# Performance work log

Hardware: AMD Instinct MI355X
Metric: run time of the kernel (lower is better)

Reference implementation:

```python
import jax, jax.numpy as jnp
import numpy as np

WINDOW = 5  # window_size from init


def _avg_pool3d(x, k):
    # Matches F.avg_pool3d(kernel=k, stride=1, padding=k//2,
    # count_include_pad=True): windowed sum with zero padding / k^3.
    pad = k // 2
    s = jax.lax.reduce_window(
        x, 0.0, jax.lax.add,
        window_dimensions=(1, 1, k, k, k),
        window_strides=(1, 1, 1, 1, 1),
        padding=[(0, 0), (0, 0), (pad, pad), (pad, pad), (pad, pad)],
    )
    return s / float(k ** 3)


def setup_inputs() -> dict:
    key = jax.random.key(0)
    k1, k2 = jax.random.split(key)
    shape = (2, 1, 160, 192, 192)  # [B, C, D, H, W]
    source = jax.random.normal(k1, shape, dtype=jnp.float32)
    target = jax.random.normal(k2, shape, dtype=jnp.float32)
    return {"source": source, "target": target}


def reference(source, target):
    conv = lambda x: _avg_pool3d(x, WINDOW)
    src_mean = conv(source)
    tgt_mean = conv(target)
    src_var = conv(source * source) - src_mean * src_mean
    tgt_var = conv(target * target) - tgt_mean * tgt_mean
    cross = conv(source * target) - src_mean * tgt_mean
    lncc = cross * cross / (src_var * tgt_var + 1e-5)
    loss = 1.0 - jnp.mean(lncc)
    return jnp.nan_to_num(loss, nan=1.0, posinf=1.0, neginf=1.0)
```

## Files before the change

### kernel.cpp

```cpp
#include <hip/hip_runtime.h>
#include <math.h>

#define W_ 192
#define H_ 192
#define D_ 160
#define B_ 2
#define TILE 16
#define HALO 20
#define CHUNK 20
#define PLANES (CHUNK + 4)
#define NTOT 11796480.0f

struct Q { float ss, tt, s2, t2, st; };

__global__ __launch_bounds__(256) void lncc_main(const float* __restrict__ src,
                                                 const float* __restrict__ tgt,
                                                 float* __restrict__ acc) {
    __shared__ float2 raw[HALO][HALO + 1];
    __shared__ float4 rs4[HALO][TILE + 1];
    __shared__ float  rs1[HALO][TILE + 1];
    __shared__ float  wsum[4];

    const int tx  = threadIdx.x, ty = threadIdx.y;
    const int tid = ty * TILE + tx;
    const int bz  = blockIdx.z;
    const int b   = bz >> 3;
    const int z0  = (bz & 7) * CHUNK;
    const int bx0 = blockIdx.x * TILE - 2;
    const int by0 = blockIdx.y * TILE - 2;

    Q r0 = {0,0,0,0,0}, r1 = {0,0,0,0,0}, r2 = {0,0,0,0,0},
      r3 = {0,0,0,0,0}, r4 = {0,0,0,0,0};
    Q zs = {0,0,0,0,0};
    float lsum = 0.0f;

    for (int i = 0; i < PLANES; ++i) {
        const int zp = z0 - 2 + i;
        Q ys = {0,0,0,0,0};
        if (zp >= 0 && zp < D_) {
            const size_t planeBase = (size_t)(b * D_ + zp) * (size_t)(H_ * W_);
            {
                int f = tid;
                #pragma unroll
                for (int rep = 0; rep < 2; ++rep, f += 256) {
                    if (f < HALO * HALO) {
                        int r  = f / HALO;
                        int c  = f - r * HALO;
                        int gy = by0 + r, gx = bx0 + c;
                        float sv = 0.0f, tv = 0.0f;
                        if ((unsigned)gx < (unsigned)W_ && (unsigned)gy < (unsigned)H_) {
                            size_t idx = planeBase + (size_t)gy * W_ + (size_t)gx;
                            sv = src[idx];
                            tv = tgt[idx];
                        }
                        raw[r][c] = make_float2(sv, tv);
                    }
                }
            }
            __syncthreads();
            {
                int p = tid;
                #pragma unroll
                for (int rep = 0; rep < 2; ++rep, p += 256) {
                    if (p < HALO * TILE) {
                        int ry = p >> 4, rx = p & 15;
                        float a0 = 0, a1 = 0, a2 = 0, a3 = 0, a4 = 0;
                        #pragma unroll
                        for (int dx = 0; dx < 5; ++dx) {
                            float2 v = raw[ry][rx + dx];
                            a0 += v.x;
                            a1 += v.y;
                            a2 = fmaf(v.x, v.x, a2);
                            a3 = fmaf(v.y, v.y, a3);
                            a4 = fmaf(v.x, v.y, a4);
                        }
                        rs4[ry][rx] = make_float4(a0, a1, a2, a3);
                        rs1[ry][rx] = a4;
                    }
                }
            }
            __syncthreads();
            #pragma unroll
            for (int dy = 0; dy < 5; ++dy) {
                float4 a = rs4[ty + dy][tx];
                float  g = rs1[ty + dy][tx];
                ys.ss += a.x;
                ys.tt += a.y;
                ys.s2 += a.z;
                ys.t2 += a.w;
                ys.st += g;
            }
        }
        zs.ss += ys.ss - r0.ss;
        zs.tt += ys.tt - r0.tt;
        zs.s2 += ys.s2 - r0.s2;
        zs.t2 += ys.t2 - r0.t2;
        zs.st += ys.st - r0.st;
        r0 = r1; r1 = r2; r2 = r3; r3 = r4; r4 = ys;

        if (i >= 4) {
            const float inv = 1.0f / 125.0f;
            float ms = zs.ss * inv, mt = zs.tt * inv;
            float vs = fmaf(-ms, ms, zs.s2 * inv);
            float vt = fmaf(-mt, mt, zs.t2 * inv);
            float cr = fmaf(-ms, mt, zs.st * inv);
            float den = fmaf(vs, vt, 1e-5f);
            lsum = fmaf(cr * cr, __builtin_amdgcn_rcpf(den), lsum);
        }
    }

    #pragma unroll
    for (int off = 32; off > 0; off >>= 1)
        lsum += __shfl_down(lsum, off, 64);
    if ((tid & 63) == 0) wsum[tid >> 6] = lsum;
    __syncthreads();
    if (tid == 0) {
        float t = wsum[0] + wsum[1] + wsum[2] + wsum[3];
        atomicAdd(acc, t);
    }
}

__global__ void lncc_zero(float* acc) { *acc = 0.0f; }

__global__ void lncc_finalize(const float* __restrict__ acc, float* __restrict__ out) {
    float loss = 1.0f - (*acc) * (1.0f / NTOT);
    if (isnan(loss) || isinf(loss)) loss = 1.0f;
    *out = loss;
}

extern "C" void kernel_launch(void* const* d_in, const int* in_sizes, int n_in,
                              void* d_out, int out_size, void* d_ws, size_t ws_size,
                              hipStream_t stream) {
    const float* src = (const float*)d_in[0];
    const float* tgt = (const float*)d_in[1];
    float* out = (float*)d_out;
    float* acc = (float*)d_ws;

    lncc_zero<<<dim3(1), dim3(1), 0, stream>>>(acc);

    dim3 grid(W_ / TILE, H_ / TILE, B_ * (D_ / CHUNK));
    dim3 block(TILE, TILE, 1);
    lncc_main<<<grid, block, 0, stream>>>(src, tgt, acc);

    lncc_finalize<<<dim3(1), dim3(1), 0, stream>>>(acc, out);
}
```

Baseline: 191.1 us.

## Double-buffer plane loads and stages, split SoA smem, replace atomic with partial sums

Restructures the per-plane loop into a software pipeline. The next plane's global loads are issued into registers while the previous plane's vertical sum and the current plane's horizontal sum run. Shared buffers are double-buffered so each plane needs one barrier instead of two. Shared arrays become structure-of-arrays, and each thread loads float2 pairs so fewer threads handle loading. The atomic accumulation and zero kernel are replaced by per-block partial sums reduced in a 256-thread finalize kernel, which removes one launch. The cost is roughly double the shared memory use, which may reduce occupancy.

```diff
diff --git a/kernel.cpp b/kernel.cpp
--- a/kernel.cpp
+++ b/kernel.cpp
@@ -7,19 +7,27 @@
 #define B_ 2
 #define TILE 16
 #define HALO 20
+#define RAWP 21
+#define RSP  17
 #define CHUNK 20
 #define PLANES (CHUNK + 4)
+#define GX 12
+#define GY 12
+#define GZ 16
+#define NBLK (GX * GY * GZ)
 #define NTOT 11796480.0f
-
-struct Q { float ss, tt, s2, t2, st; };
 
 __global__ __launch_bounds__(256) void lncc_main(const float* __restrict__ src,
                                                  const float* __restrict__ tgt,
-                                                 float* __restrict__ acc) {
-    __shared__ float2 raw[HALO][HALO + 1];
-    __shared__ float4 rs4[HALO][TILE + 1];
-    __shared__ float  rs1[HALO][TILE + 1];
-    __shared__ float  wsum[4];
+                                                 float* __restrict__ partial) {
+    __shared__ float rawS[2][HALO][RAWP];
+    __shared__ float rawT[2][HALO][RAWP];
+    __shared__ float rsS [2][HALO][RSP];
+    __shared__ float rsT [2][HALO][RSP];
+    __shared__ float rsS2[2][HALO][RSP];
+    __shared__ float rsT2[2][HALO][RSP];
+    __shared__ float rsST[2][HALO][RSP];
+    __shared__ float wsum[4];
 
     const int tx  = threadIdx.x, ty = threadIdx.y;
     const int tid = ty * TILE + tx;
@@ -29,85 +37,121 @@
     const int bx0 = blockIdx.x * TILE - 2;
     const int by0 = blockIdx.y * TILE - 2;
 
-    Q r0 = {0,0,0,0,0}, r1 = {0,0,0,0,0}, r2 = {0,0,0,0,0},
-      r3 = {0,0,0,0,0}, r4 = {0,0,0,0,0};
-    Q zs = {0,0,0,0,0};
+    const int  sr  = tid / 10;
+    const int  sc  = (tid - sr * 10) * 2;
+    const int  sgx = bx0 + sc;
+    const int  sgy = by0 + sr;
+    const bool sW  = (tid < 200);
+    const bool sOk = sW && ((unsigned)sgx < (unsigned)W_) && ((unsigned)sgy < (unsigned)H_);
+    const size_t sOff = (size_t)sgy * W_ + (size_t)sgx;
+
+    const int  p0y = tid >> 4, px = tid & 15;
+    const int  p1y = p0y + 16;
+    const bool p1  = (tid < 64);
+
+    float q0s=0,q0t=0,q0a=0,q0b=0,q0c=0;
+    float q1s=0,q1t=0,q1a=0,q1b=0,q1c=0;
+    float q2s=0,q2t=0,q2a=0,q2b=0,q2c=0;
+    float q3s=0,q3t=0,q3a=0,q3b=0,q3c=0;
+    float q4s=0,q4t=0,q4a=0,q4b=0,q4c=0;
+    float zS=0,zT=0,zS2=0,zT2=0,zST=0;
     float lsum = 0.0f;
 
-    for (int i = 0; i < PLANES; ++i) {
-        const int zp = z0 - 2 + i;
-        Q ys = {0,0,0,0,0};
-        if (zp >= 0 && zp < D_) {
-            const size_t planeBase = (size_t)(b * D_ + zp) * (size_t)(H_ * W_);
-            {
-                int f = tid;
-                #pragma unroll
-                for (int rep = 0; rep < 2; ++rep, f += 256) {
-                    if (f < HALO * HALO) {
-                        int r  = f / HALO;
-                        int c  = f - r * HALO;
-                        int gy = by0 + r, gx = bx0 + c;
-                        float sv = 0.0f, tv = 0.0f;
-                        if ((unsigned)gx < (unsigned)W_ && (unsigned)gy < (unsigned)H_) {
-                            size_t idx = planeBase + (size_t)gy * W_ + (size_t)gx;
-                            sv = src[idx];
-                            tv = tgt[idx];
-                        }
-                        raw[r][c] = make_float2(sv, tv);
-                    }
-                }
-            }
-            __syncthreads();
-            {
-                int p = tid;
-                #pragma unroll
-                for (int rep = 0; rep < 2; ++rep, p += 256) {
-                    if (p < HALO * TILE) {
-                        int ry = p >> 4, rx = p & 15;
-                        float a0 = 0, a1 = 0, a2 = 0, a3 = 0, a4 = 0;
-                        #pragma unroll
-                        for (int dx = 0; dx < 5; ++dx) {
-                            float2 v = raw[ry][rx + dx];
-                            a0 += v.x;
-                            a1 += v.y;
-                            a2 = fmaf(v.x, v.x, a2);
-                            a3 = fmaf(v.y, v.y, a3);
-                            a4 = fmaf(v.x, v.y, a4);
-                        }
-                        rs4[ry][rx] = make_float4(a0, a1, a2, a3);
-                        rs1[ry][rx] = a4;
-                    }
-                }
-            }
-            __syncthreads();
-            #pragma unroll
-            for (int dy = 0; dy < 5; ++dy) {
-                float4 a = rs4[ty + dy][tx];
-                float  g = rs1[ty + dy][tx];
-                ys.ss += a.x;
-                ys.tt += a.y;
-                ys.s2 += a.z;
-                ys.t2 += a.w;
-                ys.st += g;
-            }
+    auto phase2 = [&](int rbuf, int j) {
+        float yS=0,yT=0,yS2=0,yT2=0,yST=0;
+        #pragma unroll
+        for (int dy = 0; dy < 5; ++dy) {
+            yS  += rsS [rbuf][ty + dy][tx];
+            yT  += rsT [rbuf][ty + dy][tx];
+            yS2 += rsS2[rbuf][ty + dy][tx];
+            yT2 += rsT2[rbuf][ty + dy][tx];
+            yST += rsST[rbuf][ty + dy][tx];
         }
-        zs.ss += ys.ss - r0.ss;
-        zs.tt += ys.tt - r0.tt;
-        zs.s2 += ys.s2 - r0.s2;
-        zs.t2 += ys.t2 - r0.t2;
-        zs.st += ys.st - r0.st;
-        r0 = r1; r1 = r2; r2 = r3; r3 = r4; r4 = ys;
-
-        if (i >= 4) {
+        zS += yS - q0s;  zT += yT - q0t;  zS2 += yS2 - q0a;
+        zT2 += yT2 - q0b;  zST += yST - q0c;
+        q0s=q1s; q0t=q1t; q0a=q1a; q0b=q1b; q0c=q1c;
+        q1s=q2s; q1t=q2t; q1a=q2a; q1b=q2b; q1c=q2c;
+        q2s=q3s; q2t=q3t; q2a=q3a; q2b=q3b; q2c=q3c;
+        q3s=q4s; q3t=q4t; q3a=q4a; q3b=q4b; q3c=q4c;
+        q4s=yS;  q4t=yT;  q4a=yS2; q4b=yT2; q4c=yST;
+        if (j >= 4) {
             const float inv = 1.0f / 125.0f;
-            float ms = zs.ss * inv, mt = zs.tt * inv;
-            float vs = fmaf(-ms, ms, zs.s2 * inv);
-            float vt = fmaf(-mt, mt, zs.t2 * inv);
-            float cr = fmaf(-ms, mt, zs.st * inv);
+            float ms = zS * inv, mt = zT * inv;
+            float vs = fmaf(-ms, ms, zS2 * inv);
+            float vt = fmaf(-mt, mt, zT2 * inv);
+            float cr = fmaf(-ms, mt, zST * inv);
             float den = fmaf(vs, vt, 1e-5f);
             lsum = fmaf(cr * cr, __builtin_amdgcn_rcpf(den), lsum);
         }
+    };
+
+    {
+        float2 vS = make_float2(0.f, 0.f), vT = make_float2(0.f, 0.f);
+        const int zp = z0 - 2;
+        if (zp >= 0 && sOk) {
+            const size_t base = (size_t)(b * D_ + zp) * (size_t)(H_ * W_);
+            vS = *(const float2*)(src + base + sOff);
+            vT = *(const float2*)(tgt + base + sOff);
+        }
+        if (sW) {
+            rawS[0][sr][sc] = vS.x;  rawS[0][sr][sc + 1] = vS.y;
+            rawT[0][sr][sc] = vT.x;  rawT[0][sr][sc + 1] = vT.y;
+        }
     }
+
+    for (int i = 0; i < PLANES; ++i) {
+        const int buf = i & 1;
+        __syncthreads();
+        float2 vS = make_float2(0.f, 0.f), vT = make_float2(0.f, 0.f);
+        const bool haveNext = (i + 1 < PLANES);
+        const int  zpn = z0 - 1 + i;
+        if (haveNext && zpn >= 0 && zpn < D_ && sOk) {
+            const size_t base = (size_t)(b * D_ + zpn) * (size_t)(H_ * W_);
+            vS = *(const float2*)(src + base + sOff);
+            vT = *(const float2*)(tgt + base + sOff);
+        }
+        if (i >= 1) phase2(buf ^ 1, i - 1);
+        {
+            float a0=0,a1=0,a2=0,a3=0,a4=0;
+            #pragma unroll
+            for (int dx = 0; dx < 5; ++dx) {
+                float s = rawS[buf][p0y][px + dx];
+                float t = rawT[buf][p0y][px + dx];
+                a0 += s; a1 += t;
+                a2 = fmaf(s, s, a2);
+                a3 = fmaf(t, t, a3);
+                a4 = fmaf(s, t, a4);
+            }
+            rsS [buf][p0y][px] = a0;
+            rsT [buf][p0y][px] = a1;
+            rsS2[buf][p0y][px] = a2;
+            rsT2[buf][p0y][px] = a3;
+            rsST[buf][p0y][px] = a4;
+            if (p1) {
+                float b0=0,b1=0,b2=0,b3=0,b4=0;
+                #pragma unroll
+                for (int dx = 0; dx < 5; ++dx) {
+                    float s = rawS[buf][p1y][px + dx];
+                    float t = rawT[buf][p1y][px + dx];
+                    b0 += s; b1 += t;
+                    b2 = fmaf(s, s, b2);
+                    b3 = fmaf(t, t, b3);
+                    b4 = fmaf(s, t, b4);
+                }
+                rsS [buf][p1y][px] = b0;
+                rsT [buf][p1y][px] = b1;
+                rsS2[buf][p1y][px] = b2;
+                rsT2[buf][p1y][px] = b3;
+                rsST[buf][p1y][px] = b4;
+            }
+        }
+        if (haveNext && sW) {
+            rawS[buf ^ 1][sr][sc] = vS.x;  rawS[buf ^ 1][sr][sc + 1] = vS.y;
+            rawT[buf ^ 1][sr][sc] = vT.x;  rawT[buf ^ 1][sr][sc + 1] = vT.y;
+        }
+    }
+    __syncthreads();
+    phase2((PLANES - 1) & 1, PLANES - 1);
 
     #pragma unroll
     for (int off = 32; off > 0; off >>= 1)
@@ -115,17 +159,27 @@
     if ((tid & 63) == 0) wsum[tid >> 6] = lsum;
     __syncthreads();
     if (tid == 0) {
-        float t = wsum[0] + wsum[1] + wsum[2] + wsum[3];
-        atomicAdd(acc, t);
+        const int bid = (blockIdx.z * GY + blockIdx.y) * GX + blockIdx.x;
+        partial[bid] = wsum[0] + wsum[1] + wsum[2] + wsum[3];
     }
 }
 
-__global__ void lncc_zero(float* acc) { *acc = 0.0f; }
-
-__global__ void lncc_finalize(const float* __restrict__ acc, float* __restrict__ out) {
-    float loss = 1.0f - (*acc) * (1.0f / NTOT);
-    if (isnan(loss) || isinf(loss)) loss = 1.0f;
-    *out = loss;
+__global__ __launch_bounds__(256) void lncc_finalize(const float* __restrict__ partial,
+                                                     float* __restrict__ out) {
+    __shared__ float ws[4];
+    const int t = threadIdx.x;
+    float s = 0.0f;
+    for (int i = t; i < NBLK; i += 256) s += partial[i];
+    #pragma unroll
+    for (int off = 32; off > 0; off >>= 1) s += __shfl_down(s, off, 64);
+    if ((t & 63) == 0) ws[t >> 6] = s;
+    __syncthreads();
+    if (t == 0) {
+        float tot = ws[0] + ws[1] + ws[2] + ws[3];
+        float loss = 1.0f - tot * (1.0f / NTOT);
+        if (isnan(loss) || isinf(loss)) loss = 1.0f;
+        *out = loss;
+    }
 }
 
 extern "C" void kernel_launch(void* const* d_in, const int* in_sizes, int n_in,
@@ -134,13 +188,10 @@
     const float* src = (const float*)d_in[0];
     const float* tgt = (const float*)d_in[1];
     float* out = (float*)d_out;
-    float* acc = (float*)d_ws;
+    float* partial = (float*)d_ws;
 
-    lncc_zero<<<dim3(1), dim3(1), 0, stream>>>(acc);
-
-    dim3 grid(W_ / TILE, H_ / TILE, B_ * (D_ / CHUNK));
+    dim3 grid(GX, GY, GZ);
     dim3 block(TILE, TILE, 1);
-    lncc_main<<<grid, block, 0, stream>>>(src, tgt, acc);
-
-    lncc_finalize<<<dim3(1), dim3(1), 0, stream>>>(acc, out);
+    lncc_main<<<grid, block, 0, stream>>>(src, tgt, partial);
+    lncc_finalize<<<dim3(1), dim3(256), 0, stream>>>(partial, out);
 }
```

Result: faster. 172.3 us (-9.8%).
